# Performance work log

Hardware: AMD Instinct MI355X
Metric: run time of the kernel (lower is better)

## Reference

```python
import jax, jax.numpy as jnp
import numpy as np

GROUPS = [[0, 1, 2, 3, 4], [5, 7, 9], [6, 8, 10], [11, 13, 15], [12, 14, 16]]
G = len(GROUPS)
BN_EPS = 1e-5


def _fc_edges(n):
    r = np.repeat(np.arange(n), n)
    c = np.tile(np.arange(n), n)
    m = r != c
    return jnp.asarray(r[m]), jnp.asarray(c[m])


ROW, COL = _fc_edges(G)  # [E], E = G*(G-1) = 20


def _bn(x, scale, bias, mean, var):
    # inference-mode batchnorm over last dim
    return (x - mean) * (scale * jax.lax.rsqrt(var + BN_EPS)) + bias


def setup_inputs() -> dict:
    key = jax.random.key(0)
    ks = jax.random.split(key, 12)
    B, K, C, Ci = 4096, 17, 256, 64
    inp = {
        "x_bk_c": jax.random.normal(ks[0], (B * K, C), jnp.float32),
        "W_down": jax.random.normal(ks[1], (C, Ci), jnp.float32) * 0.05,
        "b_down": jax.random.normal(ks[2], (Ci,), jnp.float32) * 0.05,
        "bn1_scale": jax.random.uniform(ks[3], (Ci,), jnp.float32, 0.5, 1.5),
        "bn1_bias": jax.random.normal(ks[4], (Ci,), jnp.float32) * 0.1,
        "bn1_mean": jax.random.normal(ks[5], (Ci,), jnp.float32) * 0.1,
        "bn1_var": jax.random.uniform(ks[6], (Ci,), jnp.float32, 0.5, 1.5),
        "W_conv": jax.random.normal(ks[7], (Ci, 2 * Ci), jnp.float32) * 0.05,  # 1x1 conv, bias=False
        "bn2_scale": jax.random.uniform(ks[8], (Ci,), jnp.float32, 0.5, 1.5),
        "bn2_bias": jax.random.normal(ks[9], (Ci,), jnp.float32) * 0.1,
        "bn2_mean": jax.random.normal(ks[10], (Ci,), jnp.float32) * 0.1,
        "bn2_var": jax.random.uniform(ks[11], (Ci,), jnp.float32, 0.5, 1.5),
        "W_agg": jax.random.normal(jax.random.fold_in(key, 100), (Ci, C), jnp.float32) * 0.05,
        "b_agg": jax.random.normal(jax.random.fold_in(key, 101), (C,), jnp.float32) * 0.05,
        "B": B,
        "K": K,
    }
    return inp


def reference(x_bk_c, W_down, b_down, bn1_scale, bn1_bias, bn1_mean, bn1_var,
              W_conv, bn2_scale, bn2_bias, bn2_mean, bn2_var, W_agg, b_agg, B, K):
    C = x_bk_c.shape[-1]
    # down-projection + BN + SiLU
    xd = jax.nn.silu(_bn(x_bk_c @ W_down + b_down, bn1_scale, bn1_bias, bn1_mean, bn1_var))
    xd = xd.reshape(B, K, -1)  # [B, K, Ci]
    # per-group mean pooling (static small loop over 5 groups)
    means = jnp.stack([xd[:, g, :].mean(axis=1) for g in GROUPS], axis=1)  # [B, G, Ci]
    # EdgeConv over fully-connected group graph
    x_i = means[:, ROW, :]                                   # [B, E, Ci]
    x_j = means[:, COL, :]
    ef = jnp.concatenate([x_i, x_j - x_i], axis=-1)          # [B, E, 2Ci]
    pe = jax.nn.silu(_bn(ef @ W_conv.T, bn2_scale, bn2_bias, bn2_mean, bn2_var))  # [B, E, Ci]
    agg = jnp.zeros_like(means).at[:, ROW, :].add(pe)        # scatter-add over target nodes
    # per-group attention scores in C_in
    att = jax.nn.sigmoid(agg @ W_agg + b_agg)                # [B, G, C]
    # average group scores over each keypoint's memberships
    M = np.zeros((K, G), np.float32)
    for gi, g in enumerate(GROUPS):
        for kp in g:
            M[kp, gi] += 1.0
    Mj = jnp.asarray(M)
    cnt = Mj.sum(axis=1, keepdims=True)                      # [K, 1]
    ssum = jnp.einsum('kg,bgc->bkc', Mj, att)                # [B, K, C]
    safe = jnp.where(cnt > 0, cnt, 1.0)
    final = jnp.where(cnt > 0, ssum / safe, 1.0)             # ungrouped kps -> 1.0
    return (x_bk_c.reshape(B, K, C) * final).reshape(B * K, C)
```

## Files before the change

### kernel.cpp

```cpp
#include <hip/hip_runtime.h>

typedef float  v4f    __attribute__((ext_vector_type(4)));
typedef float  f32x4  __attribute__((ext_vector_type(4)));
typedef short  bf16x8 __attribute__((ext_vector_type(8)));

namespace {
constexpr int XBSTR = 264;
constexpr int XDT   = 24;
constexpr int MWC   = 129;
constexpr int ATS   = 258;
constexpr int MSTR  = 72;
constexpr int FRAG_SLOTS = 5120;

__device__ __forceinline__ float fsilu(float v){ return v/(1.f+__expf(-v)); }
__device__ __forceinline__ float fsigm(float v){ return 1.f/(1.f+__expf(-v)); }

__device__ __forceinline__ unsigned f2bf2(float a, float b){
  unsigned r;
  asm("v_cvt_pk_bf16_f32 %0, %1, %2" : "=v"(r) : "v"(a), "v"(b));
  return r;
}
__device__ __forceinline__ short f2bf(float f){
  unsigned u = __builtin_bit_cast(unsigned, f);
  return (short)((u + 0x7FFFu + ((u>>16)&1u)) >> 16);
}
__device__ __forceinline__ float bf2f(short s){
  unsigned u = ((unsigned)(unsigned short)s) << 16;
  return __builtin_bit_cast(float, u);
}

template<bool USE_WS>
__device__ __forceinline__ bf16x8 get_bd(const bf16x8* wsf, const float* Wd,
                                         int nt, int ks, int l){
  if constexpr (USE_WS) return wsf[(nt*8 + ks)*64 + l];
  bf16x8 f;
  #pragma unroll
  for (int j = 0; j < 8; ++j) f[j] = f2bf(Wd[(ks*32 + (l>>4)*8 + j)*64 + nt*16 + (l&15)]);
  return f;
}
template<bool USE_WS>
__device__ __forceinline__ bf16x8 get_bc(const bf16x8* wsf, const float* Wc,
                                         int nt, int ks, int l){
  if constexpr (USE_WS) return wsf[2048 + (nt*2 + ks)*64 + l];
  const int col = nt*16 + (l&15), cw = col>>6, co = col&63;
  bf16x8 f;
  #pragma unroll
  for (int j = 0; j < 8; ++j) f[j] = f2bf(Wc[co*128 + cw*64 + ks*32 + (l>>4)*8 + j]);
  return f;
}
template<bool USE_WS>
__device__ __forceinline__ bf16x8 get_ba(const bf16x8* wsf, const float* Wa,
                                         int nt, int ks, int l){
  if constexpr (USE_WS) return wsf[3072 + (nt*2 + ks)*64 + l];
  const int col = nt*16 + (l&15);
  bf16x8 f;
  #pragma unroll
  for (int j = 0; j < 8; ++j) f[j] = f2bf(Wa[(ks*32 + (l>>4)*8 + j)*256 + col]);
  return f;
}
}

__global__ __launch_bounds__(256)
void pack_frags(const float* __restrict__ Wd, const float* __restrict__ Wc,
                const float* __restrict__ Wa, bf16x8* __restrict__ wsf)
{
  const int e  = blockIdx.x*256 + threadIdx.x;
  const int l  = e & 63;
  const int fi = e >> 6;
  bf16x8 f;
  if (fi < 32) {
    const int nt = fi >> 3, ks = fi & 7;
    #pragma unroll
    for (int j = 0; j < 8; ++j) f[j] = f2bf(Wd[(ks*32 + (l>>4)*8 + j)*64 + nt*16 + (l&15)]);
  } else if (fi < 48) {
    const int idx = fi - 32, nt = idx >> 1, ks = idx & 1;
    const int col = nt*16 + (l&15), cw = col>>6, co = col&63;
    #pragma unroll
    for (int j = 0; j < 8; ++j) f[j] = f2bf(Wc[co*128 + cw*64 + ks*32 + (l>>4)*8 + j]);
  } else {
    const int idx = fi - 48, nt = idx >> 1, ks = idx & 1;
    const int col = nt*16 + (l&15);
    #pragma unroll
    for (int j = 0; j < 8; ++j) f[j] = f2bf(Wa[(ks*32 + (l>>4)*8 + j)*256 + col]);
  }
  wsf[e] = f;
}

template<bool USE_WS>
__global__ __launch_bounds__(256, 6)
void fused_gnn_v10(const float* __restrict__ x,
                   const float* __restrict__ Wd, const float* __restrict__ bd,
                   const float* __restrict__ bn1s, const float* __restrict__ bn1b,
                   const float* __restrict__ bn1m, const float* __restrict__ bn1v,
                   const float* __restrict__ Wc,
                   const float* __restrict__ bn2s, const float* __restrict__ bn2b,
                   const float* __restrict__ bn2m, const float* __restrict__ bn2v,
                   const float* __restrict__ Wa, const float* __restrict__ ba,
                   const bf16x8* __restrict__ wsf,
                   float* __restrict__ out)
{
  __shared__ short xbf[18*XBSTR];
  __shared__ __align__(16) char uni_raw[3072];
  __shared__ float mw[5*MWC];
  __shared__ short mbf[16*MSTR];
  __shared__ short abf[16*MSTR];

  short* xdT = (short*)uni_raw;
  short* att = (short*)uni_raw;

  const int tid  = threadIdx.x;
  const int l    = tid & 63;
  const int wv   = tid >> 6;
  const int arow = l & 15;
  const int ak8  = (l >> 4) * 8;
  const int b    = blockIdx.x;
  const int colA = wv*16 + arow;

  const float a1r = bn1s[colA] * rsqrtf(bn1v[colA] + 1e-5f);
  const float b1r = (bd[colA] - bn1m[colA])*a1r + bn1b[colA];
  const float a2r = bn2s[l] * rsqrtf(bn2v[l] + 1e-5f);
  const float b2r = bn2b[l] - bn2m[l]*a2r;

  {
    const v4f* x4 = (const v4f*)(x + (size_t)b * 4352);
    #pragma unroll
    for (int i = 0; i < 5; ++i) {
      const int idx = i*256 + tid;
      if (idx < 1088) {
        const v4f v = x4[idx];
        const int r = idx >> 6, c4 = (idx & 63) * 4;
        uint2 u; u.x = f2bf2(v.x, v.y); u.y = f2bf2(v.z, v.w);
        *(uint2*)&xbf[r*XBSTR + c4] = u;
      }
    }
  }
  __syncthreads();

  {
    f32x4 acc0 = {0.f,0.f,0.f,0.f};
    f32x4 acc1 = {0.f,0.f,0.f,0.f};
    const int rowT = (arow == 0) ? 16 : 17;
    #pragma unroll
    for (int h = 0; h < 2; ++h) {
      bf16x8 Bd[4];
      #pragma unroll
      for (int k4 = 0; k4 < 4; ++k4) Bd[k4] = get_bd<USE_WS>(wsf, Wd, wv, h*4 + k4, l);
      #pragma unroll
      for (int k4 = 0; k4 < 4; ++k4) {
        const int ks = h*4 + k4;
        bf16x8 a0 = *(const bf16x8*)&xbf[arow*XBSTR + ks*32 + ak8];
        acc0 = __builtin_amdgcn_mfma_f32_16x16x32_bf16(a0, Bd[k4], acc0, 0, 0, 0);
        bf16x8 a1 = *(const bf16x8*)&xbf[rowT*XBSTR + ks*32 + ak8];
        acc1 = __builtin_amdgcn_mfma_f32_16x16x32_bf16(a1, Bd[k4], acc1, 0, 0, 0);
      }
    }
    const float s0 = fsilu(acc0[0]*a1r + b1r);
    const float s1 = fsilu(acc0[1]*a1r + b1r);
    const float s2 = fsilu(acc0[2]*a1r + b1r);
    const float s3 = fsilu(acc0[3]*a1r + b1r);
    uint2 u; u.x = f2bf2(s0, s1); u.y = f2bf2(s2, s3);
    *(uint2*)&xdT[colA*XDT + (l>>4)*4] = u;
    if ((l >> 4) == 0)
      xdT[colA*XDT + 16] = f2bf(fsilu(acc1[0]*a1r + b1r));
  }
  __syncthreads();

  bf16x8 BcT[2][2];
  #pragma unroll
  for (int t = 0; t < 2; ++t)
    #pragma unroll
    for (int ks = 0; ks < 2; ++ks)
      BcT[t][ks] = get_bc<USE_WS>(wsf, Wc, wv*2 + t, ks, l);

  {
    const int i = l;
    #define XDV(r) bf2f(xdT[i*XDT + (r)])
    if (wv == 0) {
      const float m0 = (XDV(0)+XDV(1)+XDV(2)+XDV(3)+XDV(4))*0.2f;
      mbf[0*MSTR + i] = f2bf(m0);
      const float m4 = (XDV(12)+XDV(14)+XDV(16))*(1.f/3.f);
      mbf[4*MSTR + i] = f2bf(m4);
    } else if (wv == 1) {
      mbf[1*MSTR + i] = f2bf((XDV(5)+XDV(7)+XDV(9))*(1.f/3.f));
    } else if (wv == 2) {
      mbf[2*MSTR + i] = f2bf((XDV(6)+XDV(8)+XDV(10))*(1.f/3.f));
    } else {
      mbf[3*MSTR + i] = f2bf((XDV(11)+XDV(13)+XDV(15))*(1.f/3.f));
    }
    #undef XDV
  }
  __syncthreads();

  {
    bf16x8 am[2];
    #pragma unroll
    for (int ks = 0; ks < 2; ++ks)
      am[ks] = *(const bf16x8*)&mbf[arow*MSTR + ks*32 + ak8];
    #pragma unroll
    for (int t = 0; t < 2; ++t) {
      const int nt = wv*2 + t;
      f32x4 acc = {0.f,0.f,0.f,0.f};
      #pragma unroll
      for (int ks = 0; ks < 2; ++ks)
        acc = __builtin_amdgcn_mfma_f32_16x16x32_bf16(am[ks], BcT[t][ks], acc, 0, 0, 0);
      #pragma unroll
      for (int j = 0; j < 4; ++j) {
        const int g = (l>>4)*4 + j;
        if (g < 5) mw[g*MWC + nt*16 + arow] = acc[j];
      }
    }
  }
  __syncthreads();

  bf16x8 BaT[4][2];
  #pragma unroll
  for (int t = 0; t < 4; ++t)
    #pragma unroll
    for (int ks = 0; ks < 2; ++ks)
      BaT[t][ks] = get_ba<USE_WS>(wsf, Wa, wv*4 + t, ks, l);

  {
    const int o = l;
    float m2c[5];
    #pragma unroll
    for (int cc = 0; cc < 5; ++cc) m2c[cc] = mw[cc*MWC + 64 + o];
    auto doG = [&](int g){
      const float bse = mw[g*MWC + o] - m2c[g];
      float s = 0.f;
      #pragma unroll
      for (int cc = 0; cc < 5; ++cc) {
        if (cc != g) s += fsilu((bse + m2c[cc])*a2r + b2r);
      }
      abf[g*MSTR + o] = f2bf(s);
    };
    if (wv == 0) { doG(0); doG(4); }
    else if (wv == 1) doG(1);
    else if (wv == 2) doG(2);
    else doG(3);
  }
  __syncthreads();

  {
    bf16x8 ae[2];
    #pragma unroll
    for (int ks = 0; ks < 2; ++ks)
      ae[ks] = *(const bf16x8*)&abf[arow*MSTR + ks*32 + ak8];
    #pragma unroll
    for (int t = 0; t < 4; ++t) {
      const int nt = wv*4 + t;
      const int colE = nt*16 + arow;
      f32x4 acc = {0.f,0.f,0.f,0.f};
      #pragma unroll
      for (int ks = 0; ks < 2; ++ks)
        acc = __builtin_amdgcn_mfma_f32_16x16x32_bf16(ae[ks], BaT[t][ks], acc, 0, 0, 0);
      const float bav = ba[colE];
      #pragma unroll
      for (int j = 0; j < 4; ++j) {
        const int g = (l>>4)*4 + j;
        if (g < 5) att[g*ATS + colE] = f2bf(fsigm(acc[j] + bav));
      }
    }
  }
  __syncthreads();

  {
    const int c = tid;
    float a5[5];
    #pragma unroll
    for (int g = 0; g < 5; ++g) a5[g] = bf2f(att[g*ATS + c]);
    float* og = out + (size_t)b*4352 + c;
    constexpr int GOF[17] = {0,0,0,0,0,1,2,1,2,1,2,3,4,3,4,3,4};
    #pragma unroll
    for (int k = 0; k < 17; ++k)
      og[k*256] = bf2f(xbf[k*XBSTR + c]) * a5[GOF[k]];
  }
}

extern "C" void kernel_launch(void* const* d_in, const int* in_sizes, int n_in,
                              void* d_out, int out_size, void* d_ws, size_t ws_size,
                              hipStream_t stream) {
    (void)n_in; (void)out_size;
    const float* x   = (const float*)d_in[0];
    const float* Wd  = (const float*)d_in[1];
    const float* bd  = (const float*)d_in[2];
    const float* s1  = (const float*)d_in[3];
    const float* b1  = (const float*)d_in[4];
    const float* m1  = (const float*)d_in[5];
    const float* v1  = (const float*)d_in[6];
    const float* Wc  = (const float*)d_in[7];
    const float* s2  = (const float*)d_in[8];
    const float* b2  = (const float*)d_in[9];
    const float* m2  = (const float*)d_in[10];
    const float* v2  = (const float*)d_in[11];
    const float* Wa  = (const float*)d_in[12];
    const float* ba  = (const float*)d_in[13];

    const int Btot = in_sizes[0] / (17 * 256);
    bf16x8* wsf = (bf16x8*)d_ws;

    if (ws_size >= (size_t)FRAG_SLOTS * 16) {
        pack_frags<<<FRAG_SLOTS/256, 256, 0, stream>>>(Wd, Wc, Wa, wsf);
        fused_gnn_v10<true><<<Btot, 256, 0, stream>>>(
            x, Wd, bd, s1, b1, m1, v1, Wc, s2, b2, m2, v2, Wa, ba,
            wsf, (float*)d_out);
    } else {
        fused_gnn_v10<false><<<Btot, 256, 0, stream>>>(
            x, Wd, bd, s1, b1, m1, v1, Wc, s2, b2, m2, v2, Wa, ba,
            wsf, (float*)d_out);
    }
}
```

Measured before the change: 41.75 us.

## Process two batch items per block to reuse weight fragments

Each block now handles two consecutive batch items, with shared buffers doubled and the grid halved. Weight fragments loaded into registers (down, conv and aggregation B-operands) are reused across both items, and the global loads for both items are issued together before conversion to raise memory-level parallelism. In exchange it doubles LDS use per block, raises register pressure (launch bounds lowered to 4 blocks per SM), and assumes an even batch count.

Result: slower. 43.94 us (+5.2%).

```diff
diff --git a/kernel.cpp b/kernel.cpp
--- a/kernel.cpp
+++ b/kernel.cpp
@@ -87,8 +87,8 @@
 }
 
 template<bool USE_WS>
-__global__ __launch_bounds__(256, 6)
-void fused_gnn_v10(const float* __restrict__ x,
+__global__ __launch_bounds__(256, 4)
+void fused_gnn_v11(const float* __restrict__ x,
                    const float* __restrict__ Wd, const float* __restrict__ bd,
                    const float* __restrict__ bn1s, const float* __restrict__ bn1b,
                    const float* __restrict__ bn1m, const float* __restrict__ bn1v,
@@ -99,21 +99,18 @@
                    const bf16x8* __restrict__ wsf,
                    float* __restrict__ out)
 {
-  __shared__ short xbf[18*XBSTR];
-  __shared__ __align__(16) char uni_raw[3072];
-  __shared__ float mw[5*MWC];
-  __shared__ short mbf[16*MSTR];
-  __shared__ short abf[16*MSTR];
-
-  short* xdT = (short*)uni_raw;
-  short* att = (short*)uni_raw;
+  __shared__ short xbf[2][18*XBSTR];
+  __shared__ __align__(16) char uni_raw[2][3072];
+  __shared__ float mw[2][5*MWC];
+  __shared__ short mbf[2][16*MSTR];
+  __shared__ short abf[2][16*MSTR];
 
   const int tid  = threadIdx.x;
   const int l    = tid & 63;
   const int wv   = tid >> 6;
   const int arow = l & 15;
   const int ak8  = (l >> 4) * 8;
-  const int b    = blockIdx.x;
+  const int b0   = blockIdx.x * 2;
   const int colA = wv*16 + arow;
 
   const float a1r = bn1s[colA] * rsqrtf(bn1v[colA] + 1e-5f);
@@ -122,23 +119,35 @@
   const float b2r = bn2b[l] - bn2m[l]*a2r;
 
   {
-    const v4f* x4 = (const v4f*)(x + (size_t)b * 4352);
-    #pragma unroll
-    for (int i = 0; i < 5; ++i) {
-      const int idx = i*256 + tid;
-      if (idx < 1088) {
-        const v4f v = x4[idx];
-        const int r = idx >> 6, c4 = (idx & 63) * 4;
-        uint2 u; u.x = f2bf2(v.x, v.y); u.y = f2bf2(v.z, v.w);
-        *(uint2*)&xbf[r*XBSTR + c4] = u;
-      }
-    }
-  }
-  __syncthreads();
-
-  {
-    f32x4 acc0 = {0.f,0.f,0.f,0.f};
-    f32x4 acc1 = {0.f,0.f,0.f,0.f};
+    v4f xr[2][5];
+    #pragma unroll
+    for (int q = 0; q < 2; ++q) {
+      const v4f* x4 = (const v4f*)(x + (size_t)(b0+q) * 4352);
+      #pragma unroll
+      for (int i = 0; i < 5; ++i) {
+        const int idx = i*256 + tid;
+        if (idx < 1088) xr[q][i] = x4[idx];
+      }
+    }
+    #pragma unroll
+    for (int q = 0; q < 2; ++q) {
+      #pragma unroll
+      for (int i = 0; i < 5; ++i) {
+        const int idx = i*256 + tid;
+        if (idx < 1088) {
+          const v4f v = xr[q][i];
+          const int r = idx >> 6, c4 = (idx & 63) * 4;
+          uint2 u; u.x = f2bf2(v.x, v.y); u.y = f2bf2(v.z, v.w);
+          *(uint2*)&xbf[q][r*XBSTR + c4] = u;
+        }
+      }
+    }
+  }
+  __syncthreads();
+
+  {
+    f32x4 acc0[2] = {{0.f,0.f,0.f,0.f},{0.f,0.f,0.f,0.f}};
+    f32x4 acc1[2] = {{0.f,0.f,0.f,0.f},{0.f,0.f,0.f,0.f}};
     const int rowT = (arow == 0) ? 16 : 17;
     #pragma unroll
     for (int h = 0; h < 2; ++h) {
@@ -148,20 +157,27 @@
       #pragma unroll
       for (int k4 = 0; k4 < 4; ++k4) {
         const int ks = h*4 + k4;
-        bf16x8 a0 = *(const bf16x8*)&xbf[arow*XBSTR + ks*32 + ak8];
-        acc0 = __builtin_amdgcn_mfma_f32_16x16x32_bf16(a0, Bd[k4], acc0, 0, 0, 0);
-        bf16x8 a1 = *(const bf16x8*)&xbf[rowT*XBSTR + ks*32 + ak8];
-        acc1 = __builtin_amdgcn_mfma_f32_16x16x32_bf16(a1, Bd[k4], acc1, 0, 0, 0);
-      }
-    }
-    const float s0 = fsilu(acc0[0]*a1r + b1r);
-    const float s1 = fsilu(acc0[1]*a1r + b1r);
-    const float s2 = fsilu(acc0[2]*a1r + b1r);
-    const float s3 = fsilu(acc0[3]*a1r + b1r);
-    uint2 u; u.x = f2bf2(s0, s1); u.y = f2bf2(s2, s3);
-    *(uint2*)&xdT[colA*XDT + (l>>4)*4] = u;
-    if ((l >> 4) == 0)
-      xdT[colA*XDT + 16] = f2bf(fsilu(acc1[0]*a1r + b1r));
+        #pragma unroll
+        for (int q = 0; q < 2; ++q) {
+          bf16x8 a0 = *(const bf16x8*)&xbf[q][arow*XBSTR + ks*32 + ak8];
+          acc0[q] = __builtin_amdgcn_mfma_f32_16x16x32_bf16(a0, Bd[k4], acc0[q], 0, 0, 0);
+          bf16x8 a1 = *(const bf16x8*)&xbf[q][rowT*XBSTR + ks*32 + ak8];
+          acc1[q] = __builtin_amdgcn_mfma_f32_16x16x32_bf16(a1, Bd[k4], acc1[q], 0, 0, 0);
+        }
+      }
+    }
+    #pragma unroll
+    for (int q = 0; q < 2; ++q) {
+      short* xdT = (short*)uni_raw[q];
+      const float s0 = fsilu(acc0[q][0]*a1r + b1r);
+      const float s1 = fsilu(acc0[q][1]*a1r + b1r);
+      const float s2 = fsilu(acc0[q][2]*a1r + b1r);
+      const float s3 = fsilu(acc0[q][3]*a1r + b1r);
+      uint2 u; u.x = f2bf2(s0, s1); u.y = f2bf2(s2, s3);
+      *(uint2*)&xdT[colA*XDT + (l>>4)*4] = u;
+      if ((l >> 4) == 0)
+        xdT[colA*XDT + 16] = f2bf(fsilu(acc1[q][0]*a1r + b1r));
+    }
   }
   __syncthreads();
 
@@ -172,41 +188,46 @@
     for (int ks = 0; ks < 2; ++ks)
       BcT[t][ks] = get_bc<USE_WS>(wsf, Wc, wv*2 + t, ks, l);
 
-  {
+  #pragma unroll
+  for (int q = 0; q < 2; ++q) {
+    const short* xdT = (const short*)uni_raw[q];
     const int i = l;
     #define XDV(r) bf2f(xdT[i*XDT + (r)])
     if (wv == 0) {
-      const float m0 = (XDV(0)+XDV(1)+XDV(2)+XDV(3)+XDV(4))*0.2f;
-      mbf[0*MSTR + i] = f2bf(m0);
-      const float m4 = (XDV(12)+XDV(14)+XDV(16))*(1.f/3.f);
-      mbf[4*MSTR + i] = f2bf(m4);
+      mbf[q][0*MSTR + i] = f2bf((XDV(0)+XDV(1)+XDV(2)+XDV(3)+XDV(4))*0.2f);
+      mbf[q][4*MSTR + i] = f2bf((XDV(12)+XDV(14)+XDV(16))*(1.f/3.f));
     } else if (wv == 1) {
-      mbf[1*MSTR + i] = f2bf((XDV(5)+XDV(7)+XDV(9))*(1.f/3.f));
+      mbf[q][1*MSTR + i] = f2bf((XDV(5)+XDV(7)+XDV(9))*(1.f/3.f));
     } else if (wv == 2) {
-      mbf[2*MSTR + i] = f2bf((XDV(6)+XDV(8)+XDV(10))*(1.f/3.f));
+      mbf[q][2*MSTR + i] = f2bf((XDV(6)+XDV(8)+XDV(10))*(1.f/3.f));
     } else {
-      mbf[3*MSTR + i] = f2bf((XDV(11)+XDV(13)+XDV(15))*(1.f/3.f));
+      mbf[q][3*MSTR + i] = f2bf((XDV(11)+XDV(13)+XDV(15))*(1.f/3.f));
     }
     #undef XDV
   }
   __syncthreads();
 
   {
-    bf16x8 am[2];
-    #pragma unroll
-    for (int ks = 0; ks < 2; ++ks)
-      am[ks] = *(const bf16x8*)&mbf[arow*MSTR + ks*32 + ak8];
+    bf16x8 am[2][2];
+    #pragma unroll
+    for (int q = 0; q < 2; ++q)
+      #pragma unroll
+      for (int ks = 0; ks < 2; ++ks)
+        am[q][ks] = *(const bf16x8*)&mbf[q][arow*MSTR + ks*32 + ak8];
     #pragma unroll
     for (int t = 0; t < 2; ++t) {
       const int nt = wv*2 + t;
-      f32x4 acc = {0.f,0.f,0.f,0.f};
-      #pragma unroll
-      for (int ks = 0; ks < 2; ++ks)
-        acc = __builtin_amdgcn_mfma_f32_16x16x32_bf16(am[ks], BcT[t][ks], acc, 0, 0, 0);
-      #pragma unroll
-      for (int j = 0; j < 4; ++j) {
-        const int g = (l>>4)*4 + j;
-        if (g < 5) mw[g*MWC + nt*16 + arow] = acc[j];
+      #pragma unroll
+      for (int q = 0; q < 2; ++q) {
+        f32x4 acc = {0.f,0.f,0.f,0.f};
+        #pragma unroll
+        for (int ks = 0; ks < 2; ++ks)
+          acc = __builtin_amdgcn_mfma_f32_16x16x32_bf16(am[q][ks], BcT[t][ks], acc, 0, 0, 0);
+        #pragma unroll
+        for (int j = 0; j < 4; ++j) {
+          const int g = (l>>4)*4 + j;
+          if (g < 5) mw[q][g*MWC + nt*16 + arow] = acc[j];
+        }
       }
     }
   }
@@ -219,19 +240,20 @@
     for (int ks = 0; ks < 2; ++ks)
       BaT[t][ks] = get_ba<USE_WS>(wsf, Wa, wv*4 + t, ks, l);
 
-  {
+  #pragma unroll
+  for (int q = 0; q < 2; ++q) {
     const int o = l;
     float m2c[5];
     #pragma unroll
-    for (int cc = 0; cc < 5; ++cc) m2c[cc] = mw[cc*MWC + 64 + o];
+    for (int cc = 0; cc < 5; ++cc) m2c[cc] = mw[q][cc*MWC + 64 + o];
     auto doG = [&](int g){
-      const float bse = mw[g*MWC + o] - m2c[g];
+      const float bse = mw[q][g*MWC + o] - m2c[g];
       float s = 0.f;
       #pragma unroll
       for (int cc = 0; cc < 5; ++cc) {
         if (cc != g) s += fsilu((bse + m2c[cc])*a2r + b2r);
       }
-      abf[g*MSTR + o] = f2bf(s);
+      abf[q][g*MSTR + o] = f2bf(s);
     };
     if (wv == 0) { doG(0); doG(4); }
     else if (wv == 1) doG(1);
@@ -241,23 +263,29 @@
   __syncthreads();
 
   {
-    bf16x8 ae[2];
-    #pragma unroll
-    for (int ks = 0; ks < 2; ++ks)
-      ae[ks] = *(const bf16x8*)&abf[arow*MSTR + ks*32 + ak8];
+    bf16x8 ae[2][2];
+    #pragma unroll
+    for (int q = 0; q < 2; ++q)
+      #pragma unroll
+      for (int ks = 0; ks < 2; ++ks)
+        ae[q][ks] = *(const bf16x8*)&abf[q][arow*MSTR + ks*32 + ak8];
     #pragma unroll
     for (int t = 0; t < 4; ++t) {
       const int nt = wv*4 + t;
       const int colE = nt*16 + arow;
-      f32x4 acc = {0.f,0.f,0.f,0.f};
-      #pragma unroll
-      for (int ks = 0; ks < 2; ++ks)
-        acc = __builtin_amdgcn_mfma_f32_16x16x32_bf16(ae[ks], BaT[t][ks], acc, 0, 0, 0);
       const float bav = ba[colE];
       #pragma unroll
-      for (int j = 0; j < 4; ++j) {
-        const int g = (l>>4)*4 + j;
-        if (g < 5) att[g*ATS + colE] = f2bf(fsigm(acc[j] + bav));
+      for (int q = 0; q < 2; ++q) {
+        short* att = (short*)uni_raw[q];
+        f32x4 acc = {0.f,0.f,0.f,0.f};
+        #pragma unroll
+        for (int ks = 0; ks < 2; ++ks)
+          acc = __builtin_amdgcn_mfma_f32_16x16x32_bf16(ae[q][ks], BaT[t][ks], acc, 0, 0, 0);
+        #pragma unroll
+        for (int j = 0; j < 4; ++j) {
+          const int g = (l>>4)*4 + j;
+          if (g < 5) att[g*ATS + colE] = f2bf(fsigm(acc[j] + bav));
+        }
       }
     }
   }
@@ -265,14 +293,18 @@
 
   {
     const int c = tid;
-    float a5[5];
-    #pragma unroll
-    for (int g = 0; g < 5; ++g) a5[g] = bf2f(att[g*ATS + c]);
-    float* og = out + (size_t)b*4352 + c;
     constexpr int GOF[17] = {0,0,0,0,0,1,2,1,2,1,2,3,4,3,4,3,4};
     #pragma unroll
-    for (int k = 0; k < 17; ++k)
-      og[k*256] = bf2f(xbf[k*XBSTR + c]) * a5[GOF[k]];
+    for (int q = 0; q < 2; ++q) {
+      const short* att = (const short*)uni_raw[q];
+      float a5[5];
+      #pragma unroll
+      for (int g = 0; g < 5; ++g) a5[g] = bf2f(att[g*ATS + c]);
+      float* og = out + (size_t)(b0+q)*4352 + c;
+      #pragma unroll
+      for (int k = 0; k < 17; ++k)
+        og[k*256] = bf2f(xbf[q][k*XBSTR + c]) * a5[GOF[k]];
+    }
   }
 }
 
@@ -296,15 +328,16 @@
     const float* ba  = (const float*)d_in[13];
 
     const int Btot = in_sizes[0] / (17 * 256);
+    const int GRID = Btot / 2;
     bf16x8* wsf = (bf16x8*)d_ws;
 
     if (ws_size >= (size_t)FRAG_SLOTS * 16) {
         pack_frags<<<FRAG_SLOTS/256, 256, 0, stream>>>(Wd, Wc, Wa, wsf);
-        fused_gnn_v10<true><<<Btot, 256, 0, stream>>>(
+        fused_gnn_v11<true><<<GRID, 256, 0, stream>>>(
             x, Wd, bd, s1, b1, m1, v1, Wc, s2, b2, m2, v2, Wa, ba,
             wsf, (float*)d_out);
     } else {
-        fused_gnn_v10<false><<<Btot, 256, 0, stream>>>(
+        fused_gnn_v11<false><<<GRID, 256, 0, stream>>>(
             x, Wd, bd, s1, b1, m1, v1, Wc, s2, b2, m2, v2, Wa, ba,
             wsf, (float*)d_out);
     }
```
